# Performance work log

Hardware: AMD Instinct MI355X
Metric: run time of the kernel (lower is better)

The kernel has to match this reference:

```python
import jax, jax.numpy as jnp
import numpy as np

B = 4
NB = 8192   # points per batch
MB = 2048   # query points per batch
C_IN = 64
RADII = (0.2, 0.4)
NSAMPLES = (16, 32)
EPS = 1e-5


def setup_inputs() -> dict:
    key = jax.random.key(0)
    ks = jax.random.split(key, 8)
    inp = {}
    inp["xyz"] = jax.random.uniform(ks[0], (B * NB, 3), jnp.float32)
    inp["features"] = jax.random.normal(ks[1], (B * NB, C_IN), jnp.float32)
    inp["new_xyz"] = jax.random.uniform(ks[2], (B * MB, 3), jnp.float32)
    inp["xyz_batch_cnt"] = jnp.full((B,), NB, jnp.int32)
    inp["new_xyz_batch_cnt"] = jnp.full((B,), MB, jnp.int32)
    cin = C_IN + 3  # use_xyz=True concatenates relative xyz
    for s in range(2):
        k0, k1 = jax.random.split(ks[3 + s])
        inp[f"w{s}0"] = jax.random.normal(k0, (128, cin), jnp.float32) * (2.0 / cin) ** 0.5
        inp[f"g{s}0"] = jnp.ones((128,), jnp.float32)
        inp[f"b{s}0"] = jnp.zeros((128,), jnp.float32)
        inp[f"w{s}1"] = jax.random.normal(k1, (128, 128), jnp.float32) * (2.0 / 128) ** 0.5
        inp[f"g{s}1"] = jnp.ones((128,), jnp.float32)
        inp[f"b{s}1"] = jnp.zeros((128,), jnp.float32)
    return inp


def _ball_query(new_b, xyz_b, radius, nsample):
    # new_b: (B, M, 3), xyz_b: (B, N, 3)
    n = xyz_b.shape[1]
    # squared distances via the quadratic expansion (avoids (B,M,N,3) temp)
    d2 = (jnp.sum(new_b * new_b, -1)[:, :, None]
          + jnp.sum(xyz_b * xyz_b, -1)[:, None, :]
          - 2.0 * jnp.einsum('bmc,bnc->bmn', new_b, xyz_b))
    in_ball = d2 < radius * radius
    # first-nsample-in-original-order semantics of the CUDA ball query
    order_key = jnp.where(in_ball, jnp.arange(n, dtype=jnp.int32)[None, None, :], n)
    idxs = jnp.sort(order_key, axis=-1)[..., :nsample]        # (B, M, nsample)
    valid = idxs < n
    first = idxs[..., :1]                                     # pad with first found idx
    idx = jnp.where(valid, idxs, first)
    empty = ~valid[..., 0]                                    # no neighbor in ball
    idx = jnp.where(empty[..., None], 0, idx)
    return idx, empty


def _bn_relu(x, g, b):
    # training-mode BatchNorm2d over (M, nsample) per channel, then ReLU
    mean = jnp.mean(x, axis=(0, 1))
    var = jnp.var(x, axis=(0, 1))
    return jax.nn.relu((x - mean) * jax.lax.rsqrt(var + EPS) * g + b)


def _scale(xyz_b, feat_b, new_b, radius, nsample, w0, g0, b0, w1, g1, b1):
    idx, empty = _ball_query(new_b, xyz_b, radius, nsample)
    gather = jax.vmap(lambda pts, i: pts[i])                  # per-batch gather
    gx = gather(xyz_b, idx) - new_b[:, :, None, :]            # (B, M, ns, 3)
    gf = gather(feat_b, idx)                                  # (B, M, ns, C)
    g = jnp.concatenate([gx, gf], axis=-1)                    # use_xyz=True
    g = jnp.where(empty[..., None, None], 0.0, g)             # zero empty balls
    g = g.reshape(-1, nsample, g.shape[-1])                   # (M_total, ns, 3+C)
    h = _bn_relu(jnp.einsum('mnc,oc->mno', g, w0), g0, b0)    # shared 1x1 conv
    h = _bn_relu(jnp.einsum('mnc,oc->mno', h, w1), g1, b1)
    return jnp.max(h, axis=1)                                 # max_pool over ns


def reference(xyz, features, new_xyz, xyz_batch_cnt, new_xyz_batch_cnt,
              w00, g00, b00, w01, g01, b01,
              w10, g10, b10, w11, g11, b11):
    b = xyz_batch_cnt.shape[0]
    xyz_b = xyz.reshape(b, -1, 3)
    feat_b = features.reshape(b, -1, features.shape[-1])
    new_b = new_xyz.reshape(b, -1, 3)
    f0 = _scale(xyz_b, feat_b, new_b, RADII[0], NSAMPLES[0], w00, g00, b00, w01, g01, b01)
    f1 = _scale(xyz_b, feat_b, new_b, RADII[1], NSAMPLES[1], w10, g10, b10, w11, g11, b11)
    return new_xyz, jnp.concatenate([f0, f1], axis=1)         # (M_total, 256)
```

## Files before the change

kernel.cpp:

```cpp
#include <hip/hip_runtime.h>
#include <stdio.h>

#define NBP   8192
#define MTOT  8192
#define CIN   64
#define CO    128

#define EPR(...) do { fprintf(stderr, __VA_ARGS__); fflush(stderr); } while (0)

typedef short short8 __attribute__((ext_vector_type(8)));
typedef float floatx4 __attribute__((ext_vector_type(4)));
typedef unsigned short ushort;
typedef ushort ushort4v __attribute__((ext_vector_type(4)));

__device__ __forceinline__ ushort f2b(float f)
{
    union { unsigned int i; float f; } x; x.f = f;
    return (ushort)((x.i + 0x7fffu + ((x.i >> 16) & 1u)) >> 16);
}
__device__ __forceinline__ float b2f(ushort u)
{
    union { unsigned int i; float f; } x; x.i = ((unsigned int)u) << 16;
    return x.f;
}
__device__ __forceinline__ void split_rne(float v, ushort& h, ushort& l)
{
    ushort hh = f2b(v);
    h = hh; l = f2b(v - b2f(hh));
}

__global__ void __launch_bounds__(256, 1) StackSAModuleMSG_85761906966880_kernel(
    const float* __restrict__ xyz, const float* __restrict__ nxyz,
    float* __restrict__ out, float* __restrict__ stats,
    const float* __restrict__ feat, ushort* __restrict__ fh,
    int* __restrict__ idx0, int* __restrict__ idx1,
    int* __restrict__ empty0, int* __restrict__ empty1,
    const float* __restrict__ w00, const float* __restrict__ w01,
    const float* __restrict__ w10, const float* __restrict__ w11,
    ushort* __restrict__ wh00, ushort* __restrict__ wl00,
    ushort* __restrict__ wh01, ushort* __restrict__ wl01,
    ushort* __restrict__ wh10, ushort* __restrict__ wl10,
    ushort* __restrict__ wh11, ushort* __restrict__ wl11)
{
    if (blockIdx.x < MTOT/4) {
        const double r2a = 0.2 * 0.2;
        const double r2b = 0.4 * 0.4;
        int m    = blockIdx.x * 4 + (threadIdx.x >> 6);
        int lane = threadIdx.x & 63;
        int b    = m >> 11;
        int base = b * NBP;

        double nx = (double)nxyz[3*m+0];
        double ny = (double)nxyz[3*m+1];
        double nz = (double)nxyz[3*m+2];
        double nn = nx*nx + ny*ny + nz*nz;

        int cnt0 = 0, cnt1 = 0;
        int first0 = base, first1 = base;
        unsigned long long lt = (1ull << lane) - 1ull;

        for (int j = 0; j < NBP; j += 64) {
            int gi = base + j + lane;
            double px = (double)xyz[3*gi+0];
            double py = (double)xyz[3*gi+1];
            double pz = (double)xyz[3*gi+2];
            double pp = px*px + py*py + pz*pz;
            double dt = nx*px + ny*py + nz*pz;
            double d2 = nn + pp - 2.0*dt;
            bool in0 = d2 < r2a;
            bool in1 = d2 < r2b;
            unsigned long long m0 = __ballot(in0);
            unsigned long long m1 = __ballot(in1);
            if (in0) {
                int p0 = cnt0 + __popcll(m0 & lt);
                if (p0 < 16) idx0[m*16 + p0] = gi;
            }
            if (in1) {
                int p1 = cnt1 + __popcll(m1 & lt);
                if (p1 < 32) idx1[m*32 + p1] = gi;
            }
            if (cnt0 == 0 && m0) first0 = base + j + (__ffsll((long long)m0) - 1);
            if (cnt1 == 0 && m1) first1 = base + j + (__ffsll((long long)m1) - 1);
            cnt0 += __popcll(m0);
            cnt1 += __popcll(m1);
            if (cnt0 >= 16 && cnt1 >= 32) break;
        }
        int c0 = cnt0 < 16 ? cnt0 : 16;
        int c1 = cnt1 < 32 ? cnt1 : 32;
        if (lane >= c0 && lane < 16) idx0[m*16 + lane] = first0;
        if (lane >= c1 && lane < 32) idx1[m*32 + lane] = first1;
        if (lane == 0) { empty0[m] = (cnt0 == 0); empty1[m] = (cnt1 == 0); }
    } else {
        int i = (blockIdx.x - MTOT/4) * 256 + threadIdx.x;
        if (i < 1024) stats[i] = 0.f;
        if (i < MTOT*3) out[i] = nxyz[i];
        if (i < 128*128) {
            split_rne(w01[i], wh01[i], wl01[i]);
            split_rne(w11[i], wh11[i], wl11[i]);
        }
        if (i < 128*96) {
            int o = i / 96, kd = i - o*96;
            int c = (kd < 64) ? (kd + 3) : ((kd < 67) ? (kd - 64) : -1);
            float a = (c >= 0) ? w00[o*67 + c] : 0.f;
            split_rne(a, wh00[i], wl00[i]);
            float b = (c >= 0) ? w10[o*67 + c] : 0.f;
            split_rne(b, wh10[i], wl10[i]);
        }
        {
            float4 v = *(const float4*)(feat + (size_t)4*i);
            ushort4v h;
            h[0] = f2b(v.x); h[1] = f2b(v.y); h[2] = f2b(v.z); h[3] = f2b(v.w);
            *(ushort4v*)(fh + (size_t)4*i) = h;
        }
    }
}

template<int NS, int GM>
__device__ __forceinline__ void stats1_body(
    const ushort* __restrict__ fh,
    const float* __restrict__ xyz, const float* __restrict__ nxyz,
    const int* __restrict__ idx, const int* __restrict__ empty,
    const ushort* __restrict__ wh0, float* __restrict__ part,
    int bx, int t, ushort* ah)
{
    int m0 = bx * GM;
    int wv = t >> 6, lane = t & 63, l16 = lane & 15, qo = lane >> 4;
    int n0 = 32*wv;

    short8 bh[3][2];
#pragma unroll
    for (int ks = 0; ks < 3; ks++)
#pragma unroll
        for (int nt = 0; nt < 2; nt++)
            bh[ks][nt] = *(const short8*)(wh0 +
                (long long)(n0 + 16*nt + l16)*96 + ks*32 + qo*8);

    unsigned em = 0;
#pragma unroll
    for (int g = 0; g < GM; g++) em |= (empty[m0 + g] ? 1u : 0u) << g;
    const long long ib = (long long)m0 * NS;
    int n1 = t >> 3, c8 = t & 7, n2 = n1 + 32;
    int n3 = t >> 2, k3 = t & 3;
    int gi1 = idx[ib + n1];
    int gi2 = idx[ib + n2];
    short8 vh1 = *(const short8*)(fh + (size_t)gi1*CIN + 8*c8);
    short8 vh2 = *(const short8*)(fh + (size_t)gi2*CIN + 8*c8);
    const short8 Z8 = {0,0,0,0,0,0,0,0};
    short8 vh3 = Z8;
    int g3 = n3 / NS;
    if (k3 == 0 && !((em >> g3) & 1u)) {
        int gi3 = idx[ib + n3];
#pragma unroll
        for (int c = 0; c < 3; c++)
            vh3[c] = (short)f2b(xyz[3*gi3+c] - nxyz[3*(m0+g3)+c]);
    }

    if ((em >> (n1 / NS)) & 1u) vh1 = Z8;
    if ((em >> (n2 / NS)) & 1u) vh2 = Z8;
    *(short8*)(ah + n1*136 + 8*c8) = vh1;
    *(short8*)(ah + n2*136 + 8*c8) = vh2;
    *(short8*)(ah + n3*136 + 64 + 8*k3) = vh3;
    __syncthreads();

    floatx4 acc[4][2];
#pragma unroll
    for (int i = 0; i < 4; i++) {
        acc[i][0] = (floatx4){0.f,0.f,0.f,0.f};
        acc[i][1] = (floatx4){0.f,0.f,0.f,0.f};
    }
#pragma unroll
    for (int ks = 0; ks < 3; ks++) {
        int kb = ks*32 + qo*8;
#pragma unroll
        for (int mt = 0; mt < 4; mt++) {
            int ao = (16*mt + l16)*136 + kb;
            short8 fh8 = *(const short8*)(ah + ao);
#pragma unroll
            for (int nt = 0; nt < 2; nt++)
                acc[mt][nt] = __builtin_amdgcn_mfma_f32_16x16x32_bf16(
                                  fh8, bh[ks][nt], acc[mt][nt], 0, 0, 0);
        }
    }

    float sum[2] = {0.f,0.f}, sq[2] = {0.f,0.f};
#pragma unroll
    for (int mt = 0; mt < 4; mt++)
#pragma unroll
        for (int nt = 0; nt < 2; nt++)
#pragma unroll
            for (int r = 0; r < 4; r++) {
                float a = acc[mt][nt][r];
                sum[nt] += a; sq[nt] = fmaf(a, a, sq[nt]);
            }
#pragma unroll
    for (int nt = 0; nt < 2; nt++) {
        sum[nt] += __shfl_xor(sum[nt], 16); sum[nt] += __shfl_xor(sum[nt], 32);
        sq[nt]  += __shfl_xor(sq[nt],  16); sq[nt]  += __shfl_xor(sq[nt],  32);
    }
    if (lane < 16) {
#pragma unroll
        for (int nt = 0; nt < 2; nt++) {
            int c = n0 + 16*nt + lane;
            part[(long long)bx*256 + c]       = sum[nt];
            part[(long long)bx*256 + 128 + c] = sq[nt];
        }
    }
}

__global__ void __launch_bounds__(256, 4) sa_stats1_both(
    const ushort* __restrict__ fh,
    const float* __restrict__ xyz, const float* __restrict__ nxyz,
    const int* __restrict__ idx0, const int* __restrict__ empty0,
    const ushort* __restrict__ wh00, float* __restrict__ partA,
    const int* __restrict__ idx1, const int* __restrict__ empty1,
    const ushort* __restrict__ wh10, float* __restrict__ partB)
{
    __shared__ ushort ah[64*136];
    int t = threadIdx.x;
    if (blockIdx.x < MTOT/4)
        stats1_body<16,4>(fh, xyz, nxyz, idx0, empty0, wh00, partA,
                          blockIdx.x, t, ah);
    else
        stats1_body<32,2>(fh, xyz, nxyz, idx1, empty1, wh10, partB,
                          blockIdx.x - MTOT/4, t, ah);
}

template<int NS, int GM>
__device__ __forceinline__ void fused_body(
    const ushort* __restrict__ fh,
    const float* __restrict__ xyz, const float* __restrict__ nxyz,
    const int* __restrict__ idx, const int* __restrict__ empty,
    const ushort* __restrict__ wh0, const ushort* __restrict__ wl0,
    const ushort* __restrict__ wh1, const ushort* __restrict__ wl1,
    const float* __restrict__ g0, const float* __restrict__ b0,
    const float* __restrict__ s1sum, const float* __restrict__ s1sq,
    float* __restrict__ part, float* __restrict__ mxo, float* __restrict__ mno,
    float invN, int bx, int t,
    ushort* ah, float* kv, float* sv)
{
    const int TPG = NS/16;
    int m0 = bx * GM;
    int wv = t >> 6, lane = t & 63, l16 = lane & 15, qo = lane >> 4;
    int n0 = 32*wv;

    if (t < 128) {
        float mean = s1sum[t] * invN;
        float var  = s1sq[t] * invN - mean * mean;
        float k    = rsqrtf(var + 1e-5f) * g0[t];
        kv[t] = k;
        sv[t] = b0[t] - mean * k;
    }

    short8 b1h[3][2], b1l[3][2];
#pragma unroll
    for (int ks = 0; ks < 3; ks++)
#pragma unroll
        for (int nt = 0; nt < 2; nt++) {
            long long wo = (long long)(n0 + 16*nt + l16)*96 + ks*32 + qo*8;
            b1h[ks][nt] = *(const short8*)(wh0 + wo);
            b1l[ks][nt] = *(const short8*)(wl0 + wo);
        }

    unsigned em = 0;
#pragma unroll
    for (int g = 0; g < GM; g++) em |= (empty[m0 + g] ? 1u : 0u) << g;
    const long long ib = (long long)m0 * NS;
    int n1 = t >> 3, c8 = t & 7, n2 = n1 + 32;
    int n3 = t >> 2, k3 = t & 3;
    int gi1 = idx[ib + n1];
    int gi2 = idx[ib + n2];
    short8 vh1 = *(const short8*)(fh + (size_t)gi1*CIN + 8*c8);
    short8 vh2 = *(const short8*)(fh + (size_t)gi2*CIN + 8*c8);
    const short8 Z8 = {0,0,0,0,0,0,0,0};
    short8 vh3 = Z8;
    int g3 = n3 / NS;
    if (k3 == 0 && !((em >> g3) & 1u)) {
        int gi3 = idx[ib + n3];
#pragma unroll
        for (int c = 0; c < 3; c++)
            vh3[c] = (short)f2b(xyz[3*gi3+c] - nxyz[3*(m0+g3)+c]);
    }

    if ((em >> (n1 / NS)) & 1u) vh1 = Z8;
    if ((em >> (n2 / NS)) & 1u) vh2 = Z8;
    *(short8*)(ah + n1*136 + 8*c8) = vh1;
    *(short8*)(ah + n2*136 + 8*c8) = vh2;
    *(short8*)(ah + n3*136 + 64 + 8*k3) = vh3;
    __syncthreads();

    {
        floatx4 acc[4][2];
#pragma unroll
        for (int i = 0; i < 4; i++) {
            acc[i][0] = (floatx4){0.f,0.f,0.f,0.f};
            acc[i][1] = (floatx4){0.f,0.f,0.f,0.f};
        }
#pragma unroll
        for (int ks = 0; ks < 3; ks++) {
            int kb = ks*32 + qo*8;
#pragma unroll
            for (int mt = 0; mt < 4; mt++) {
                int ao = (16*mt + l16)*136 + kb;
                short8 fh8 = *(const short8*)(ah + ao);
#pragma unroll
                for (int nt = 0; nt < 2; nt++) {
                    acc[mt][nt] = __builtin_amdgcn_mfma_f32_16x16x32_bf16(
                                      fh8, b1l[ks][nt], acc[mt][nt], 0, 0, 0);
                    acc[mt][nt] = __builtin_amdgcn_mfma_f32_16x16x32_bf16(
                                      fh8, b1h[ks][nt], acc[mt][nt], 0, 0, 0);
                }
            }
        }

        __syncthreads();
#pragma unroll
        for (int nt = 0; nt < 2; nt++) {
            int c = n0 + 16*nt + l16;
            float k = kv[c], s = sv[c];
#pragma unroll
            for (int mt = 0; mt < 4; mt++) {
                int rbase = 16*mt + qo*4;
#pragma unroll
                for (int r = 0; r < 4; r += 2) {
                    float h0 = fmaxf(fmaf(acc[mt][nt][r],   k, s), 0.f);
                    float h1 = fmaxf(fmaf(acc[mt][nt][r+1], k, s), 0.f);
                    unsigned int pk;
                    asm("v_cvt_pk_bf16_f32 %0, %1, %2"
                        : "=v"(pk) : "v"(h0), "v"(h1));
                    ah[(rbase + r    )*136 + c] = (ushort)(pk & 0xffffu);
                    ah[(rbase + r + 1)*136 + c] = (ushort)(pk >> 16);
                }
            }
        }

        short8 b2h[4][2], b2l[4][2];
#pragma unroll
        for (int ks = 0; ks < 4; ks++)
#pragma unroll
            for (int nt = 0; nt < 2; nt++) {
                long long wo = (long long)(n0 + 16*nt + l16)*128 + ks*32 + qo*8;
                b2h[ks][nt] = *(const short8*)(wh1 + wo);
                b2l[ks][nt] = *(const short8*)(wl1 + wo);
            }
        __syncthreads();

        floatx4 acc2[4][2];
#pragma unroll
        for (int i = 0; i < 4; i++) {
            acc2[i][0] = (floatx4){0.f,0.f,0.f,0.f};
            acc2[i][1] = (floatx4){0.f,0.f,0.f,0.f};
        }
#pragma unroll
        for (int ks = 0; ks < 4; ks++) {
            int kb = ks*32 + qo*8;
#pragma unroll
            for (int mt = 0; mt < 4; mt++) {
                int ao = (16*mt + l16)*136 + kb;
                short8 fh8 = *(const short8*)(ah + ao);
#pragma unroll
                for (int nt = 0; nt < 2; nt++) {
                    acc2[mt][nt] = __builtin_amdgcn_mfma_f32_16x16x32_bf16(
                                      fh8, b2l[ks][nt], acc2[mt][nt], 0, 0, 0);
                    acc2[mt][nt] = __builtin_amdgcn_mfma_f32_16x16x32_bf16(
                                      fh8, b2h[ks][nt], acc2[mt][nt], 0, 0, 0);
                }
            }
        }

        float sum[2] = {0.f,0.f}, sq[2] = {0.f,0.f};
        float Mx[GM][2], Mn[GM][2];
#pragma unroll
        for (int g = 0; g < GM; g++) {
            Mx[g][0] = -3.4e38f; Mx[g][1] = -3.4e38f;
            Mn[g][0] =  3.4e38f; Mn[g][1] =  3.4e38f;
        }
#pragma unroll
        for (int mt = 0; mt < 4; mt++) {
            int gg = mt / TPG;
#pragma unroll
            for (int nt = 0; nt < 2; nt++)
#pragma unroll
                for (int r = 0; r < 4; r++) {
                    float a = acc2[mt][nt][r];
                    sum[nt] += a; sq[nt] = fmaf(a, a, sq[nt]);
                    Mx[gg][nt] = fmaxf(Mx[gg][nt], a);
                    Mn[gg][nt] = fminf(Mn[gg][nt], a);
                }
        }
#pragma unroll
        for (int nt = 0; nt < 2; nt++) {
            sum[nt] += __shfl_xor(sum[nt], 16); sum[nt] += __shfl_xor(sum[nt], 32);
            sq[nt]  += __shfl_xor(sq[nt],  16); sq[nt]  += __shfl_xor(sq[nt],  32);
#pragma unroll
            for (int g = 0; g < GM; g++) {
                Mx[g][nt] = fmaxf(Mx[g][nt], __shfl_xor(Mx[g][nt], 16));
                Mx[g][nt] = fmaxf(Mx[g][nt], __shfl_xor(Mx[g][nt], 32));
                Mn[g][nt] = fminf(Mn[g][nt], __shfl_xor(Mn[g][nt], 16));
                Mn[g][nt] = fminf(Mn[g][nt], __shfl_xor(Mn[g][nt], 32));
            }
        }
        if (lane < 16) {
#pragma unroll
            for (int nt = 0; nt < 2; nt++) {
                int c = n0 + 16*nt + lane;
                part[(long long)bx*256 + c]       = sum[nt];
                part[(long long)bx*256 + 128 + c] = sq[nt];
#pragma unroll
                for (int g = 0; g < GM; g++) {
                    mxo[(long long)(m0+g)*128 + c] = Mx[g][nt];
                    mno[(long long)(m0+g)*128 + c] = Mn[g][nt];
                }
            }
        }
    }
}

__global__ void __launch_bounds__(256, 4) sa_fused_both(
    const ushort* __restrict__ fh,
    const float* __restrict__ xyz, const float* __restrict__ nxyz,
    const int* __restrict__ idx0, const int* __restrict__ empty0,
    const ushort* __restrict__ wh00, const ushort* __restrict__ wl00,
    const ushort* __restrict__ wh01, const ushort* __restrict__ wl01,
    const float* __restrict__ g00, const float* __restrict__ b00,
    const float* __restrict__ s1sumA, const float* __restrict__ s1sqA,
    float* __restrict__ partA, float* __restrict__ mx0, float* __restrict__ mn0,
    float invN0,
    const int* __restrict__ idx1, const int* __restrict__ empty1,
    const ushort* __restrict__ wh10, const ushort* __restrict__ wl10,
    const ushort* __restrict__ wh11, const ushort* __restrict__ wl11,
    const float* __restrict__ g10, const float* __restrict__ b10,
    const float* __restrict__ s1sumB, const float* __restrict__ s1sqB,
    float* __restrict__ partB, float* __restrict__ mx1, float* __restrict__ mn1,
    float invN1)
{
    __shared__ ushort ah[64*136];
    __shared__ float kv[128], sv[128];
    int t = threadIdx.x;
    if (blockIdx.x < MTOT/4)
        fused_body<16,4>(fh, xyz, nxyz, idx0, empty0,
                         wh00, wl00, wh01, wl01, g00, b00, s1sumA, s1sqA,
                         partA, mx0, mn0, invN0, blockIdx.x, t,
                         ah, kv, sv);
    else
        fused_body<32,2>(fh, xyz, nxyz, idx1, empty1,
                         wh10, wl10, wh11, wl11, g10, b10, s1sumB, s1sqB,
                         partB, mx1, mn1, invN1, blockIdx.x - MTOT/4, t,
                         ah, kv, sv);
}

__global__ void __launch_bounds__(256, 1) sa_reduce2(
    const float* __restrict__ partA, int nbA, float* __restrict__ dstA,
    const float* __restrict__ partB, int nbB, float* __restrict__ dstB)
{
    __shared__ float red[256];
    int t = threadIdx.x;
    const float* part; float* dst; int nb, b;
    if (blockIdx.x < 256) { part = partA; dst = dstA; nb = nbA; b = blockIdx.x; }
    else                  { part = partB; dst = dstB; nb = nbB; b = blockIdx.x - 256; }
    float s = 0.f;
    for (int i = t; i < nb; i += 256) s += part[(long long)i*256 + b];
    red[t] = s;
    __syncthreads();
    for (int off = 128; off > 0; off >>= 1) {
        if (t < off) red[t] += red[t + off];
        __syncthreads();
    }
    if (t == 0) dst[b] = red[0];
}

__global__ void __launch_bounds__(256, 1) sa_pass3b(
    const float* __restrict__ mx0, const float* __restrict__ mn0,
    const float* __restrict__ g01, const float* __restrict__ b01,
    const float* __restrict__ mx1, const float* __restrict__ mn1,
    const float* __restrict__ g11, const float* __restrict__ b11,
    const float* __restrict__ stats, float* __restrict__ outp,
    float invN0, float invN1)
{
    int i = blockIdx.x * 256 + threadIdx.x;
    int m = i >> 8, o = i & 255;
    bool sc1 = o >= 128;
    int oc = o & 127;
    const float* sm = sc1 ? (stats + 768) : (stats + 256);
    const float* sp = sc1 ? (stats + 896) : (stats + 384);
    float invN = sc1 ? invN1 : invN0;
    float gg   = sc1 ? g11[oc] : g01[oc];
    float bb   = sc1 ? b11[oc] : b01[oc];
    float mean = sm[oc] * invN;
    float var  = sp[oc] * invN - mean * mean;
    float k    = rsqrtf(var + 1e-5f) * gg;
    float sh   = bb - mean * k;
    long long mi = (long long)m * 128 + oc;
    float v;
    if (k >= 0.f) v = sc1 ? mx1[mi] : mx0[mi];
    else          v = sc1 ? mn1[mi] : mn0[mi];
    float r = fmaf(v, k, sh);
    outp[i] = r > 0.f ? r : 0.f;
}

extern "C" void kernel_launch(void* const* d_in, const int* in_sizes, int n_in,
                              void* d_out, int out_size, void* d_ws, size_t ws_size,
                              hipStream_t stream)
{
    const float* xyz  = (const float*)d_in[0];
    const float* feat = (const float*)d_in[1];
    const float* nxyz = (const float*)d_in[2];
    const float* w00 = (const float*)d_in[5];
    const float* g00 = (const float*)d_in[6];
    const float* b00 = (const float*)d_in[7];
    const float* w01 = (const float*)d_in[8];
    const float* g01 = (const float*)d_in[9];
    const float* b01 = (const float*)d_in[10];
    const float* w10 = (const float*)d_in[11];
    const float* g10 = (const float*)d_in[12];
    const float* b10 = (const float*)d_in[13];
    const float* w11 = (const float*)d_in[14];
    const float* g11 = (const float*)d_in[15];
    const float* b11 = (const float*)d_in[16];
    float* out = (float*)d_out;

    char*  wsb    = (char*)d_ws;
    float* stats  = (float*)(wsb);
    int*   idx0   = (int*)(wsb + 4096);
    int*   idx1   = (int*)(wsb + 4096 + 524288);
    int*   empty0 = (int*)(wsb + 4096 + 524288 + 1048576);
    int*   empty1 = (int*)(wsb + 4096 + 524288 + 1048576 + 32768);
    ushort* fh    = (ushort*)(wsb + 2000000);
    float* mx0    = (float*)(wsb + 150000000);
    float* mn0    = (float*)(wsb + 155000000);
    float* mx1    = (float*)(wsb + 160000000);
    float* mn1    = (float*)(wsb + 165000000);
    ushort* wh01  = (ushort*)(wsb + 170000000);
    ushort* wl01  = (ushort*)(wsb + 171000000);
    ushort* wh11  = (ushort*)(wsb + 172000000);
    ushort* wl11  = (ushort*)(wsb + 173000000);
    ushort* wh00  = (ushort*)(wsb + 174000000);
    ushort* wl00  = (ushort*)(wsb + 175000000);
    ushort* wh10  = (ushort*)(wsb + 176000000);
    ushort* wl10  = (ushort*)(wsb + 177000000);
    float* partA  = (float*)(wsb + 180000000);
    float* partB  = (float*)(wsb + 183000000);

    const float invN0 = 1.0f / (float)(MTOT*16);
    const float invN1 = 1.0f / (float)(MTOT*32);
    float* fout = out + MTOT*3;

    StackSAModuleMSG_85761906966880_kernel<<<MTOT/4 + 2048, 256, 0, stream>>>(
        xyz, nxyz, out, stats, feat, fh,
        idx0, idx1, empty0, empty1,
        w00, w01, w10, w11,
        wh00, wl00, wh01, wl01, wh10, wl10, wh11, wl11);

    sa_stats1_both<<<MTOT/4 + MTOT/2, 256, 0, stream>>>(
        fh, xyz, nxyz,
        idx0, empty0, wh00, partA,
        idx1, empty1, wh10, partB);

    sa_reduce2<<<512, 256, 0, stream>>>(partA, MTOT/4, stats + 0,
                                        partB, MTOT/2, stats + 512);

    sa_fused_both<<<MTOT/4 + MTOT/2, 256, 0, stream>>>(
        fh, xyz, nxyz,
        idx0, empty0, wh00, wl00, wh01, wl01, g00, b00,
        stats + 0, stats + 128, partA, mx0, mn0, invN0,
        idx1, empty1, wh10, wl10, wh11, wl11, g10, b10,
        stats + 512, stats + 640, partB, mx1, mn1, invN1);

    sa_reduce2<<<512, 256, 0, stream>>>(partA, MTOT/4, stats + 256,
                                        partB, MTOT/2, stats + 768);

    sa_pass3b<<<(MTOT*256)/256, 256, 0, stream>>>(
        mx0, mn0, g01, b01, mx1, mn1, g11, b11, stats, fout, invN0, invN1);

    hipError_t e = hipGetLastError();
    if (e != hipSuccess) EPR("[KL] enqueue err=%d (%s)\n", (int)e, hipGetErrorString(e));
}
```

Measured before the change: 234.9 us.

## Double stats-pass tile rows and use separate LDS buffer for hidden activations

The first statistics kernel now processes 128 gathered rows per block instead of 64, halving the block count and the number of partial-sum rows the reduction reads, while amortizing weight-fragment loads. Each wave now holds 8x2 MFMA accumulators, which raises register pressure. The fused kernel writes the layer-1 activations into a separate LDS buffer instead of reusing the input tile, which removes a block-wide barrier but doubles that kernel's LDS footprint and may reduce occupancy.

```diff
diff --git a/kernel.cpp b/kernel.cpp
--- a/kernel.cpp
+++ b/kernel.cpp
@@ -123,6 +123,7 @@
     const ushort* __restrict__ wh0, float* __restrict__ part,
     int bx, int t, ushort* ah)
 {
+    constexpr int ROWS = NS*GM;
     int m0 = bx * GM;
     int wv = t >> 6, lane = t & 63, l16 = lane & 15, qo = lane >> 4;
     int n0 = 32*wv;
@@ -134,6 +135,135 @@
         for (int nt = 0; nt < 2; nt++)
             bh[ks][nt] = *(const short8*)(wh0 +
                 (long long)(n0 + 16*nt + l16)*96 + ks*32 + qo*8);
+
+    unsigned em = 0;
+#pragma unroll
+    for (int g = 0; g < GM; g++) em |= (empty[m0 + g] ? 1u : 0u) << g;
+    const long long ib = (long long)m0 * NS;
+    const short8 Z8 = {0,0,0,0,0,0,0,0};
+#pragma unroll
+    for (int e = t; e < ROWS*8; e += 256) {
+        int n = e >> 3, c8 = e & 7;
+        int gi = idx[ib + n];
+        short8 v = *(const short8*)(fh + (size_t)gi*CIN + 8*c8);
+        if ((em >> (n / NS)) & 1u) v = Z8;
+        *(short8*)(ah + n*136 + 8*c8) = v;
+    }
+#pragma unroll
+    for (int e = t; e < ROWS*4; e += 256) {
+        int n = e >> 2, k3 = e & 3;
+        short8 v = Z8;
+        if (k3 == 0) {
+            int g = n / NS;
+            if (!((em >> g) & 1u)) {
+                int gi = idx[ib + n];
+#pragma unroll
+                for (int c = 0; c < 3; c++)
+                    v[c] = (short)f2b(xyz[3*gi+c] - nxyz[3*(m0+g)+c]);
+            }
+        }
+        *(short8*)(ah + n*136 + 64 + 8*k3) = v;
+    }
+    __syncthreads();
+
+    floatx4 acc[8][2];
+#pragma unroll
+    for (int i = 0; i < 8; i++) {
+        acc[i][0] = (floatx4){0.f,0.f,0.f,0.f};
+        acc[i][1] = (floatx4){0.f,0.f,0.f,0.f};
+    }
+#pragma unroll
+    for (int ks = 0; ks < 3; ks++) {
+        int kb = ks*32 + qo*8;
+#pragma unroll
+        for (int mt = 0; mt < 8; mt++) {
+            int ao = (16*mt + l16)*136 + kb;
+            short8 fh8 = *(const short8*)(ah + ao);
+#pragma unroll
+            for (int nt = 0; nt < 2; nt++)
+                acc[mt][nt] = __builtin_amdgcn_mfma_f32_16x16x32_bf16(
+                                  fh8, bh[ks][nt], acc[mt][nt], 0, 0, 0);
+        }
+    }
+
+    float sum[2] = {0.f,0.f}, sq[2] = {0.f,0.f};
+#pragma unroll
+    for (int mt = 0; mt < 8; mt++)
+#pragma unroll
+        for (int nt = 0; nt < 2; nt++)
+#pragma unroll
+            for (int r = 0; r < 4; r++) {
+                float a = acc[mt][nt][r];
+                sum[nt] += a; sq[nt] = fmaf(a, a, sq[nt]);
+            }
+#pragma unroll
+    for (int nt = 0; nt < 2; nt++) {
+        sum[nt] += __shfl_xor(sum[nt], 16); sum[nt] += __shfl_xor(sum[nt], 32);
+        sq[nt]  += __shfl_xor(sq[nt],  16); sq[nt]  += __shfl_xor(sq[nt],  32);
+    }
+    if (lane < 16) {
+#pragma unroll
+        for (int nt = 0; nt < 2; nt++) {
+            int c = n0 + 16*nt + lane;
+            part[(long long)bx*256 + c]       = sum[nt];
+            part[(long long)bx*256 + 128 + c] = sq[nt];
+        }
+    }
+}
+
+__global__ void __launch_bounds__(256, 4) sa_stats1_both(
+    const ushort* __restrict__ fh,
+    const float* __restrict__ xyz, const float* __restrict__ nxyz,
+    const int* __restrict__ idx0, const int* __restrict__ empty0,
+    const ushort* __restrict__ wh00, float* __restrict__ partA,
+    const int* __restrict__ idx1, const int* __restrict__ empty1,
+    const ushort* __restrict__ wh10, float* __restrict__ partB)
+{
+    __shared__ ushort ah[128*136];
+    int t = threadIdx.x;
+    if (blockIdx.x < MTOT/8)
+        stats1_body<16,8>(fh, xyz, nxyz, idx0, empty0, wh00, partA,
+                          blockIdx.x, t, ah);
+    else
+        stats1_body<32,4>(fh, xyz, nxyz, idx1, empty1, wh10, partB,
+                          blockIdx.x - MTOT/8, t, ah);
+}
+
+template<int NS, int GM>
+__device__ __forceinline__ void fused_body(
+    const ushort* __restrict__ fh,
+    const float* __restrict__ xyz, const float* __restrict__ nxyz,
+    const int* __restrict__ idx, const int* __restrict__ empty,
+    const ushort* __restrict__ wh0, const ushort* __restrict__ wl0,
+    const ushort* __restrict__ wh1, const ushort* __restrict__ wl1,
+    const float* __restrict__ g0, const float* __restrict__ b0,
+    const float* __restrict__ s1sum, const float* __restrict__ s1sq,
+    float* __restrict__ part, float* __restrict__ mxo, float* __restrict__ mno,
+    float invN, int bx, int t,
+    ushort* ah, ushort* hb, float* kv, float* sv)
+{
+    const int TPG = NS/16;
+    int m0 = bx * GM;
+    int wv = t >> 6, lane = t & 63, l16 = lane & 15, qo = lane >> 4;
+    int n0 = 32*wv;
+
+    if (t < 128) {
+        float mean = s1sum[t] * invN;
+        float var  = s1sq[t] * invN - mean * mean;
+        float k    = rsqrtf(var + 1e-5f) * g0[t];
+        kv[t] = k;
+        sv[t] = b0[t] - mean * k;
+    }
+
+    short8 b1h[3][2], b1l[3][2];
+#pragma unroll
+    for (int ks = 0; ks < 3; ks++)
+#pragma unroll
+        for (int nt = 0; nt < 2; nt++) {
+            long long wo = (long long)(n0 + 16*nt + l16)*96 + ks*32 + qo*8;
+            b1h[ks][nt] = *(const short8*)(wh0 + wo);
+            b1l[ks][nt] = *(const short8*)(wl0 + wo);
+        }
 
     unsigned em = 0;
 #pragma unroll
@@ -162,132 +292,6 @@
     *(short8*)(ah + n3*136 + 64 + 8*k3) = vh3;
     __syncthreads();
 
-    floatx4 acc[4][2];
-#pragma unroll
-    for (int i = 0; i < 4; i++) {
-        acc[i][0] = (floatx4){0.f,0.f,0.f,0.f};
-        acc[i][1] = (floatx4){0.f,0.f,0.f,0.f};
-    }
-#pragma unroll
-    for (int ks = 0; ks < 3; ks++) {
-        int kb = ks*32 + qo*8;
-#pragma unroll
-        for (int mt = 0; mt < 4; mt++) {
-            int ao = (16*mt + l16)*136 + kb;
-            short8 fh8 = *(const short8*)(ah + ao);
-#pragma unroll
-            for (int nt = 0; nt < 2; nt++)
-                acc[mt][nt] = __builtin_amdgcn_mfma_f32_16x16x32_bf16(
-                                  fh8, bh[ks][nt], acc[mt][nt], 0, 0, 0);
-        }
-    }
-
-    float sum[2] = {0.f,0.f}, sq[2] = {0.f,0.f};
-#pragma unroll
-    for (int mt = 0; mt < 4; mt++)
-#pragma unroll
-        for (int nt = 0; nt < 2; nt++)
-#pragma unroll
-            for (int r = 0; r < 4; r++) {
-                float a = acc[mt][nt][r];
-                sum[nt] += a; sq[nt] = fmaf(a, a, sq[nt]);
-            }
-#pragma unroll
-    for (int nt = 0; nt < 2; nt++) {
-        sum[nt] += __shfl_xor(sum[nt], 16); sum[nt] += __shfl_xor(sum[nt], 32);
-        sq[nt]  += __shfl_xor(sq[nt],  16); sq[nt]  += __shfl_xor(sq[nt],  32);
-    }
-    if (lane < 16) {
-#pragma unroll
-        for (int nt = 0; nt < 2; nt++) {
-            int c = n0 + 16*nt + lane;
-            part[(long long)bx*256 + c]       = sum[nt];
-            part[(long long)bx*256 + 128 + c] = sq[nt];
-        }
-    }
-}
-
-__global__ void __launch_bounds__(256, 4) sa_stats1_both(
-    const ushort* __restrict__ fh,
-    const float* __restrict__ xyz, const float* __restrict__ nxyz,
-    const int* __restrict__ idx0, const int* __restrict__ empty0,
-    const ushort* __restrict__ wh00, float* __restrict__ partA,
-    const int* __restrict__ idx1, const int* __restrict__ empty1,
-    const ushort* __restrict__ wh10, float* __restrict__ partB)
-{
-    __shared__ ushort ah[64*136];
-    int t = threadIdx.x;
-    if (blockIdx.x < MTOT/4)
-        stats1_body<16,4>(fh, xyz, nxyz, idx0, empty0, wh00, partA,
-                          blockIdx.x, t, ah);
-    else
-        stats1_body<32,2>(fh, xyz, nxyz, idx1, empty1, wh10, partB,
-                          blockIdx.x - MTOT/4, t, ah);
-}
-
-template<int NS, int GM>
-__device__ __forceinline__ void fused_body(
-    const ushort* __restrict__ fh,
-    const float* __restrict__ xyz, const float* __restrict__ nxyz,
-    const int* __restrict__ idx, const int* __restrict__ empty,
-    const ushort* __restrict__ wh0, const ushort* __restrict__ wl0,
-    const ushort* __restrict__ wh1, const ushort* __restrict__ wl1,
-    const float* __restrict__ g0, const float* __restrict__ b0,
-    const float* __restrict__ s1sum, const float* __restrict__ s1sq,
-    float* __restrict__ part, float* __restrict__ mxo, float* __restrict__ mno,
-    float invN, int bx, int t,
-    ushort* ah, float* kv, float* sv)
-{
-    const int TPG = NS/16;
-    int m0 = bx * GM;
-    int wv = t >> 6, lane = t & 63, l16 = lane & 15, qo = lane >> 4;
-    int n0 = 32*wv;
-
-    if (t < 128) {
-        float mean = s1sum[t] * invN;
-        float var  = s1sq[t] * invN - mean * mean;
-        float k    = rsqrtf(var + 1e-5f) * g0[t];
-        kv[t] = k;
-        sv[t] = b0[t] - mean * k;
-    }
-
-    short8 b1h[3][2], b1l[3][2];
-#pragma unroll
-    for (int ks = 0; ks < 3; ks++)
-#pragma unroll
-        for (int nt = 0; nt < 2; nt++) {
-            long long wo = (long long)(n0 + 16*nt + l16)*96 + ks*32 + qo*8;
-            b1h[ks][nt] = *(const short8*)(wh0 + wo);
-            b1l[ks][nt] = *(const short8*)(wl0 + wo);
-        }
-
-    unsigned em = 0;
-#pragma unroll
-    for (int g = 0; g < GM; g++) em |= (empty[m0 + g] ? 1u : 0u) << g;
-    const long long ib = (long long)m0 * NS;
-    int n1 = t >> 3, c8 = t & 7, n2 = n1 + 32;
-    int n3 = t >> 2, k3 = t & 3;
-    int gi1 = idx[ib + n1];
-    int gi2 = idx[ib + n2];
-    short8 vh1 = *(const short8*)(fh + (size_t)gi1*CIN + 8*c8);
-    short8 vh2 = *(const short8*)(fh + (size_t)gi2*CIN + 8*c8);
-    const short8 Z8 = {0,0,0,0,0,0,0,0};
-    short8 vh3 = Z8;
-    int g3 = n3 / NS;
-    if (k3 == 0 && !((em >> g3) & 1u)) {
-        int gi3 = idx[ib + n3];
-#pragma unroll
-        for (int c = 0; c < 3; c++)
-            vh3[c] = (short)f2b(xyz[3*gi3+c] - nxyz[3*(m0+g3)+c]);
-    }
-
-    if ((em >> (n1 / NS)) & 1u) vh1 = Z8;
-    if ((em >> (n2 / NS)) & 1u) vh2 = Z8;
-    *(short8*)(ah + n1*136 + 8*c8) = vh1;
-    *(short8*)(ah + n2*136 + 8*c8) = vh2;
-    *(short8*)(ah + n3*136 + 64 + 8*k3) = vh3;
-    __syncthreads();
-
     {
         floatx4 acc[4][2];
 #pragma unroll
@@ -312,7 +316,6 @@
             }
         }
 
-        __syncthreads();
 #pragma unroll
         for (int nt = 0; nt < 2; nt++) {
             int c = n0 + 16*nt + l16;
@@ -327,8 +330,8 @@
                     unsigned int pk;
                     asm("v_cvt_pk_bf16_f32 %0, %1, %2"
                         : "=v"(pk) : "v"(h0), "v"(h1));
-                    ah[(rbase + r    )*136 + c] = (ushort)(pk & 0xffffu);
-                    ah[(rbase + r + 1)*136 + c] = (ushort)(pk >> 16);
+                    hb[(rbase + r    )*136 + c] = (ushort)(pk & 0xffffu);
+                    hb[(rbase + r + 1)*136 + c] = (ushort)(pk >> 16);
                 }
             }
         }
@@ -356,7 +359,7 @@
 #pragma unroll
             for (int mt = 0; mt < 4; mt++) {
                 int ao = (16*mt + l16)*136 + kb;
-                short8 fh8 = *(const short8*)(ah + ao);
+                short8 fh8 = *(const short8*)(hb + ao);
 #pragma unroll
                 for (int nt = 0; nt < 2; nt++) {
                     acc2[mt][nt] = __builtin_amdgcn_mfma_f32_16x16x32_bf16(
@@ -434,18 +437,19 @@
     float invN1)
 {
     __shared__ ushort ah[64*136];
+    __shared__ ushort hb[64*136];
     __shared__ float kv[128], sv[128];
     int t = threadIdx.x;
     if (blockIdx.x < MTOT/4)
         fused_body<16,4>(fh, xyz, nxyz, idx0, empty0,
                          wh00, wl00, wh01, wl01, g00, b00, s1sumA, s1sqA,
                          partA, mx0, mn0, invN0, blockIdx.x, t,
-                         ah, kv, sv);
+                         ah, hb, kv, sv);
     else
         fused_body<32,2>(fh, xyz, nxyz, idx1, empty1,
                          wh10, wl10, wh11, wl11, g10, b10, s1sumB, s1sqB,
                          partB, mx1, mn1, invN1, blockIdx.x - MTOT/4, t,
-                         ah, kv, sv);
+                         ah, hb, kv, sv);
 }
 
 __global__ void __launch_bounds__(256, 1) sa_reduce2(
@@ -550,13 +554,13 @@
         w00, w01, w10, w11,
         wh00, wl00, wh01, wl01, wh10, wl10, wh11, wl11);
 
-    sa_stats1_both<<<MTOT/4 + MTOT/2, 256, 0, stream>>>(
+    sa_stats1_both<<<MTOT/8 + MTOT/4, 256, 0, stream>>>(
         fh, xyz, nxyz,
         idx0, empty0, wh00, partA,
         idx1, empty1, wh10, partB);
 
-    sa_reduce2<<<512, 256, 0, stream>>>(partA, MTOT/4, stats + 0,
-                                        partB, MTOT/2, stats + 512);
+    sa_reduce2<<<512, 256, 0, stream>>>(partA, MTOT/8, stats + 0,
+                                        partB, MTOT/4, stats + 512);
 
     sa_fused_both<<<MTOT/4 + MTOT/2, 256, 0, stream>>>(
         fh, xyz, nxyz,
```

Measured after the change: 232.0 us. About the same (-1.3%).
